# Optimization experiments

Hardware: AMD Instinct MI355X
Metric: run time of the kernel (lower is better)

## Reference

```python
import jax, jax.numpy as jnp
import numpy as np

T, B, DIM, N = 2048, 16, 1024, 64


def setup_inputs() -> dict:
    key = jax.random.key(0)
    ks = jax.random.split(key, 6)
    # xavier-uniform-ish scale for [N, DIM] linear weights
    lim = float(np.sqrt(6.0 / (DIM + N)))
    mk = lambda k: jax.random.uniform(k, (N, DIM), jnp.float32, -lim, lim)
    return {
        "x": jax.random.normal(ks[0], (T, B, DIM), jnp.float32),
        "S": jnp.zeros((B, N, N), jnp.float32),
        "W_k": mk(ks[1]),
        "W_v": mk(ks[2]),
        "W_q": mk(ks[3]),
        "W_alpha": mk(ks[4]),
        "d_alpha": jnp.full((N,), 0.1, jnp.float32),
        "b_alpha": jnp.full((N,), 2.0, jnp.float32),
    }


def reference(x, S, W_k, W_v, W_q, W_alpha, d_alpha, b_alpha):
    # Projections for the whole sequence at once: [T, B, N]
    k_all = jnp.einsum('tbd,nd->tbn', x, W_k)
    v_all = jnp.einsum('tbd,nd->tbn', x, W_v)
    q_all = jnp.einsum('tbd,nd->tbn', x, W_q)
    a_all = jnp.einsum('tbd,nd->tbn', x, W_alpha)

    def step(S, inp):
        k, v, q, ax = inp  # each [B, N]
        retrieved = jnp.einsum('bij,bj->bi', S, k)                 # [B, N]
        alpha = jax.nn.sigmoid(ax + d_alpha * retrieved + b_alpha)  # [B, N]
        outer_vk = v[:, :, None] * k[:, None, :]                    # [B, N, N]
        S = alpha[:, :, None] * S + (1.0 - alpha[:, :, None]) * outer_vk
        out = jnp.einsum('bij,bj->bi', S, q)                        # [B, N]
        out = out * jax.nn.silu(out)
        return S, out

    S_final, output = jax.lax.scan(step, S, (k_all, v_all, q_all, a_all))
    return output, S_final
```

## Files before the change

kernel.cpp:

```cpp
#include <hip/hip_runtime.h>
#include <hip/hip_bf16.h>

#define T_STEPS 2048
#define BATCH 16
#define DIM 1024
#define NDIM 64
#define M_TOTAL (T_STEPS * BATCH)
#define STRIDE (BATCH * NDIM)
#define CH 32
#define NC (T_STEPS / CH)

typedef __attribute__((ext_vector_type(8))) short bf16x8;
typedef __attribute__((ext_vector_type(4))) float f32x4;
typedef __attribute__((ext_vector_type(2))) float f32x2;

#define NEG_LOG2E -1.44269504088896f

__device__ inline unsigned pk_bf(float lo, float hi) {
    __hip_bfloat162 h = __float22bfloat162_rn(float2{lo, hi});
    return *(unsigned*)&h;
}

template <int CTRL>
__device__ inline float dpp_add(float x) {
    int v = __builtin_amdgcn_update_dpp(0, __float_as_int(x), CTRL, 0xF, 0xF, true);
    return x + __int_as_float(v);
}
__device__ inline float red16(float x) {
    x = dpp_add<0xB1>(x);
    x = dpp_add<0x4E>(x);
    x = dpp_add<0x141>(x);
    x = dpp_add<0x140>(x);
    return x;
}
__device__ inline void red16x2(float& a, float& b) {
    a = dpp_add<0xB1>(a);  b = dpp_add<0xB1>(b);
    a = dpp_add<0x4E>(a);  b = dpp_add<0x4E>(b);
    a = dpp_add<0x141>(a); b = dpp_add<0x141>(b);
    a = dpp_add<0x140>(a); b = dpp_add<0x140>(b);
}
__device__ inline float silu_o(float o) {
    float e = __builtin_amdgcn_exp2f(o * NEG_LOG2E);
    return o * o * __builtin_amdgcn_rcpf(1.f + e);
}

#define AS1 __attribute__((address_space(1)))
#define AS3 __attribute__((address_space(3)))
__device__ inline void gl_lds16(const float* g, float* l) {
    __builtin_amdgcn_global_load_lds((const AS1 unsigned*)g, (AS3 unsigned*)l, 16, 0, 0);
}
__device__ inline void gl_lds16s(const unsigned short* g, unsigned short* l) {
    __builtin_amdgcn_global_load_lds((const AS1 unsigned*)g, (AS3 unsigned*)l, 16, 0, 0);
}
__device__ inline void gl_lds4(const float* g, float* l) {
    __builtin_amdgcn_global_load_lds((const AS1 unsigned*)g, (AS3 unsigned*)l, 4, 0, 0);
}
#define WAIT_VM0 do { __builtin_amdgcn_s_waitcnt(0x0F70); asm volatile("" ::: "memory"); } while (0)

__global__ __launch_bounds__(256) void pack_w(
    const float* __restrict__ Wk, const float* __restrict__ Wq,
    const float* __restrict__ Wv, const float* __restrict__ Wa,
    unsigned short* __restrict__ Wb) {
    int n = blockIdx.x;
    int sel = n >> 6;
    const float* W = (sel == 0) ? Wk : (sel == 1) ? Wq : (sel == 2) ? Wv : Wa;
    int k4 = threadIdx.x * 4;
    float4 f = *(const float4*)(W + (size_t)(n & 63) * DIM + k4);
    uint2 u;
    u.x = pk_bf(f.x, f.y);
    u.y = pk_bf(f.z, f.w);
    *(uint2*)(Wb + (size_t)n * DIM + k4) = u;
}

__global__ __launch_bounds__(256, 2) void proj_kernel(
    const float* __restrict__ x, const unsigned short* __restrict__ Wb,
    const float* __restrict__ ba, float* __restrict__ Kp, float* __restrict__ Qp,
    float* __restrict__ VAi) {
    __shared__ float sA[128 * 64];
    __shared__ unsigned short sB[128 * 64];

    const int m0 = blockIdx.x * 128;
    const int ntile = blockIdx.y;
    const int tid = threadIdx.x;
    const int wv = tid >> 6, lane = tid & 63, lrow = lane & 15, quad = lane >> 4;
    const int wm = wv & 1, wn = wv >> 1;

    f32x4 acc[4][4];
#pragma unroll
    for (int a = 0; a < 4; a++)
#pragma unroll
        for (int b = 0; b < 4; b++) acc[a][b] = (f32x4)(0.f);

    const float* xg = x + (size_t)(m0 + (tid >> 4)) * DIM + (tid & 15) * 4;
    const unsigned short* wg = Wb + (size_t)(ntile * 128 + (tid >> 3)) * DIM + (tid & 7) * 8;

    for (int it = 0; it < 16; ++it) {
        const int k0 = it * 64;
        __syncthreads();
#pragma unroll
        for (int j = 0; j < 8; ++j)
            gl_lds16(xg + (size_t)(16 * j) * DIM + k0, &sA[(tid + 256 * j) * 4]);
#pragma unroll
        for (int j = 0; j < 4; ++j)
            gl_lds16s(wg + (size_t)(32 * j) * DIM + k0, &sB[(tid + 256 * j) * 8]);
        WAIT_VM0;
        __syncthreads();

#pragma unroll
        for (int ks = 0; ks < 2; ++ks) {
            bf16x8 af[4];
#pragma unroll
            for (int mt = 0; mt < 4; ++mt) {
                const float* pa = &sA[(wm * 64 + mt * 16 + lrow) * 64 + ks * 32 + quad * 8];
                float4 lo = ((const float4*)pa)[0], hi = ((const float4*)pa)[1];
                unsigned pk[4] = {pk_bf(lo.x, lo.y), pk_bf(lo.z, lo.w),
                                  pk_bf(hi.x, hi.y), pk_bf(hi.z, hi.w)};
                af[mt] = *(bf16x8*)pk;
            }
#pragma unroll
            for (int nt = 0; nt < 4; ++nt) {
                bf16x8 bfr = *(const bf16x8*)&sB[(wn * 64 + nt * 16 + lrow) * 64 + ks * 32 + quad * 8];
#pragma unroll
                for (int mt = 0; mt < 4; ++mt)
                    acc[mt][nt] = __builtin_amdgcn_mfma_f32_16x16x32_bf16(af[mt], bfr, acc[mt][nt], 0, 0, 0);
            }
        }
    }

    const int g2 = ntile * 2 + wn;
    float bav[4];
    if (g2 == 3) {
#pragma unroll
        for (int nt = 0; nt < 4; ++nt) bav[nt] = ba[nt * 16 + lrow];
    }
#pragma unroll
    for (int mt = 0; mt < 4; ++mt)
#pragma unroll
        for (int nt = 0; nt < 4; ++nt) {
            int col = nt * 16 + lrow;
#pragma unroll
            for (int reg = 0; reg < 4; ++reg) {
                int m = m0 + wm * 64 + mt * 16 + quad * 4 + reg;
                float vvv = acc[mt][nt][reg];
                if (g2 == 0) Kp[(size_t)m * 64 + col] = vvv;
                else if (g2 == 1) Qp[(size_t)m * 64 + col] = vvv;
                else if (g2 == 2) VAi[(size_t)m * 128 + col * 2] = vvv;
                else VAi[(size_t)m * 128 + col * 2 + 1] = NEG_LOG2E * (vvv + bav[nt]);
            }
        }
}

__global__ __launch_bounds__(256) void kq_kernel(
    const float* __restrict__ Kp, const float* __restrict__ Qp,
    float* __restrict__ kq, float* __restrict__ kk) {
    int m = blockIdx.x * 16 + (threadIdx.x >> 4);
    int c = threadIdx.x & 15;
    float4 k = *(const float4*)(Kp + (size_t)m * 64 + c * 4);
    float4 q = *(const float4*)(Qp + (size_t)m * 64 + c * 4);
    float4 kn = {0.f, 0.f, 0.f, 0.f};
    if (m + BATCH < M_TOTAL) kn = *(const float4*)(Kp + (size_t)(m + BATCH) * 64 + c * 4);
    float pq = k.x * q.x + k.y * q.y + k.z * q.z + k.w * q.w;
    float pk = k.x * kn.x + k.y * kn.y + k.z * kn.z + k.w * kn.w;
    red16x2(pq, pk);
    if (c == 0) { kq[m] = pq; kk[m] = pk; }
}

__global__ __launch_bounds__(64, 1) void recur_kernel(
    const float* __restrict__ Kp, const float* __restrict__ Qp,
    const float* __restrict__ VAi, const float* __restrict__ KQp,
    const float* __restrict__ KKp,
    const float* __restrict__ S0, const float* __restrict__ d_alpha,
    float* __restrict__ out, float* __restrict__ Sout) {
    __shared__ float Kl[2][CH][64];
    __shared__ float Ql[2][CH][64];
    __shared__ float VAl[2][CH][8];
    __shared__ float KQl[2][64];
    __shared__ float KKl[2][64];
    __shared__ float OlT[4][CH];

    int b = blockIdx.y, g = blockIdx.x, lane = threadIdx.x;
    int r = lane >> 4, c = lane & 15, i = g * 4 + r, c4 = c * 4;

    f32x4 sv = *(const f32x4*)(S0 + ((size_t)b * NDIM + i) * NDIM + c4);
    float da2 = d_alpha[i] * NEG_LOG2E;

    const float* Kbase = Kp + (size_t)b * NDIM + (size_t)(lane >> 4) * STRIDE + (lane & 15) * 4;
    const float* Qbase = Qp + (size_t)b * NDIM + (size_t)(lane >> 4) * STRIDE + (lane & 15) * 4;
    const float* VAbase = VAi + (size_t)b * 128 + g * 8 + (lane & 1) * 4 + (size_t)(lane >> 1) * 2048;
    const float* KQbase = KQp + b + (size_t)(lane & 31) * BATCH;
    const float* KKbase = KKp + b + (size_t)(lane & 31) * BATCH;

    auto load_chunk = [&](int t0, int buf) {
#pragma unroll
        for (int j = 0; j < 8; ++j) {
            gl_lds16(Kbase + (size_t)(t0 + j * 4) * STRIDE, &Kl[buf][j * 4][0]);
            gl_lds16(Qbase + (size_t)(t0 + j * 4) * STRIDE, &Ql[buf][j * 4][0]);
        }
        gl_lds16(VAbase + (size_t)t0 * 2048, &VAl[buf][0][0]);
        gl_lds4(KQbase + (size_t)t0 * BATCH, &KQl[buf][0]);
        gl_lds4(KKbase + (size_t)t0 * BATCH, &KKl[buf][0]);
    };

    f32x4 kg[2][4], qg[2][4], kqg[2], kkg[2];
    f32x2 vg[2][4];
    f32x4 og;
    float ee, ckm, rqm, vkk, vkq, v_cur;

#define LOADG(gi, buf, t4_) do {                                          \
    const float* Kb_ = &Kl[buf][0][0] + (t4_) * 64 + c4;                  \
    const float* Qb_ = &Ql[buf][0][0] + (t4_) * 64 + c4;                  \
    _Pragma("unroll")                                                     \
    for (int u_ = 0; u_ < 4; ++u_) {                                      \
        kg[gi][u_] = *(const f32x4*)(Kb_ + u_ * 64);                      \
        qg[gi][u_] = *(const f32x4*)(Qb_ + u_ * 64);                      \
        vg[gi][u_] = *(const f32x2*)(&VAl[buf][0][0] + ((t4_) + u_) * 8 + r * 2); \
    }                                                                     \
    kqg[gi] = *(const f32x4*)(&KQl[buf][0] + (t4_));                      \
    kkg[gi] = *(const f32x4*)(&KKl[buf][0] + (t4_));                      \
} while (0)

#define STEP(u, kt_, kt2_, qt1_, vt1_, kqt1_, kkt1_) do {                 \
    float alpha_ = __builtin_amdgcn_rcpf(1.f + ee);                       \
    float rk1_ = fmaf(alpha_, ckm, vkk);                 \
    ee = __builtin_amdgcn_exp2f(fmaf(da2, rk1_, (vt1_).y));               \
    float o_ = fmaf(alpha_, rqm, vkq);                       \
    f32x4 w_ = v_cur * (kt_);                                             \
    f32x4 d_ = sv - w_;                                                   \
    sv = w_ + alpha_ * d_;                                       \
    f32x2 pq_ = (qt1_).lo * sv.lo; pq_ = (qt1_).hi * sv.hi + pq_;         \
    f32x2 pk_ = (kt2_).lo * sv.lo; pk_ = (kt2_).hi * sv.hi + pk_;         \
    float rq_ = pq_.x + pq_.y, ck_ = pk_.x + pk_.y;                       \
    red16x2(rq_, ck_);                                  \
    float v1_ = (vt1_).x;                                                 \
    vkq = v1_ * (kqt1_); vkk = v1_ * (kkt1_);                             \
    rqm = rq_ - vkq; ckm = ck_ - vkk;                                     \
    og[u] = o_;                                                           \
    v_cur = v1_;                                                          \
} while (0)

#define GROUP_A() do {                                                          \
    STEP(0, kg[0][0], kg[0][2], qg[0][1], vg[0][1], kqg[0][1], kkg[0][1]);      \
    STEP(1, kg[0][1], kg[0][3], qg[0][2], vg[0][2], kqg[0][2], kkg[0][2]);      \
    STEP(2, kg[0][2], kg[1][0], qg[0][3], vg[0][3], kqg[0][3], kkg[0][3]);      \
    STEP(3, kg[0][3], kg[1][1], qg[1][0], vg[1][0], kqg[1][0], kkg[1][0]);      \
} while (0)
#define GROUP_B() do {                                                          \
    STEP(0, kg[1][0], kg[1][2], qg[1][1], vg[1][1], kqg[1][1], kkg[1][1]);      \
    STEP(1, kg[1][1], kg[1][3], qg[1][2], vg[1][2], kqg[1][2], kkg[1][2]);      \
    STEP(2, kg[1][2], kg[0][0], qg[1][3], vg[1][3], kqg[1][3], kkg[1][3]);      \
    STEP(3, kg[1][3], kg[0][1], qg[0][0], vg[0][0], kqg[0][0], kkg[0][0]);      \
} while (0)

    load_chunk(0, 0);
    WAIT_VM0;
    LOADG(0, 0, 0);
    {
        f32x2 p0 = kg[0][0].lo * sv.lo; p0 = kg[0][0].hi * sv.hi + p0;
        f32x2 p1 = qg[0][0].lo * sv.lo; p1 = qg[0][0].hi * sv.hi + p1;
        f32x2 p2 = kg[0][1].lo * sv.lo; p2 = kg[0][1].hi * sv.hi + p2;
        float rk0 = p0.x + p0.y, rq0 = p1.x + p1.y, ck0 = p2.x + p2.y;
        red16x2(rk0, rq0);
        ck0 = red16(ck0);
        float v0 = vg[0][0].x;
        ee = __builtin_amdgcn_exp2f(fmaf(da2, rk0, vg[0][0].y));
        vkq = v0 * kqg[0][0];
        vkk = v0 * kkg[0][0];
        rqm = rq0 - vkq;
        ckm = ck0 - vkk;
        v_cur = v0;
    }

#pragma unroll 1
    for (int j = 0; j < NC; ++j) {
        const int cb = j & 1, nb = cb ^ 1;
        if (j + 1 < NC) load_chunk((j + 1) * CH, nb);

#pragma unroll 1
        for (int t8 = 0; t8 < 24; t8 += 8) {
            LOADG(1, cb, t8 + 4);
            GROUP_A();
            if (c == 0) *(f32x4*)(&OlT[r][t8]) = og;
            LOADG(0, cb, t8 + 8);
            GROUP_B();
            if (c == 0) *(f32x4*)(&OlT[r][t8 + 4]) = og;
        }
        LOADG(1, cb, 28);
        GROUP_A();
        if (c == 0) *(f32x4*)(&OlT[r][24]) = og;
        WAIT_VM0;
        LOADG(0, nb, 0);
        GROUP_B();
        if (c == 0) *(f32x4*)(&OlT[r][28]) = og;

        if (lane < 32) {
            float4 t4o;
            t4o.x = silu_o(OlT[0][lane]);
            t4o.y = silu_o(OlT[1][lane]);
            t4o.z = silu_o(OlT[2][lane]);
            t4o.w = silu_o(OlT[3][lane]);
            *(float4*)(out + ((size_t)(j * CH + lane) * BATCH + b) * NDIM + g * 4) = t4o;
        }
    }
#undef GROUP_A
#undef GROUP_B
#undef STEP
#undef LOADG

    *(float4*)(Sout + ((size_t)b * NDIM + i) * NDIM + c4) = float4{sv.x, sv.y, sv.z, sv.w};
}

extern "C" void kernel_launch(void* const* d_in, const int* in_sizes, int n_in,
                              void* d_out, int out_size, void* d_ws, size_t ws_size,
                              hipStream_t stream) {
    const float* x  = (const float*)d_in[0];
    const float* S0 = (const float*)d_in[1];
    const float* Wk = (const float*)d_in[2];
    const float* Wv = (const float*)d_in[3];
    const float* Wq = (const float*)d_in[4];
    const float* Wa = (const float*)d_in[5];
    const float* da = (const float*)d_in[6];
    const float* ba = (const float*)d_in[7];

    float* out = (float*)d_out;
    float* Sout = out + (size_t)T_STEPS * BATCH * NDIM;

    const size_t per = (size_t)M_TOTAL * NDIM;
    float* Kp  = (float*)d_ws;
    float* Qp  = Kp + per;
    float* VAi = Qp + per;
    float* kq  = VAi + 2 * per;
    float* kk  = kq + M_TOTAL;
    unsigned short* Wb = (unsigned short*)(kk + M_TOTAL);

    pack_w<<<dim3(256), dim3(256), 0, stream>>>(Wk, Wq, Wv, Wa, Wb);
    proj_kernel<<<dim3(M_TOTAL / 128, 2), dim3(256), 0, stream>>>(x, Wb, ba, Kp, Qp, VAi);
    kq_kernel<<<dim3(M_TOTAL / 16), dim3(256), 0, stream>>>(Kp, Qp, kq, kk);
    recur_kernel<<<dim3(16, BATCH), dim3(64), 0, stream>>>(Kp, Qp, VAi, kq, kk, S0, da, out, Sout);
}
```

Measured before the change: 446.1 us.

## Widen projection tile to all four weights and defer output reduction in recurrence

The projection kernel now computes all 256 output columns per block, one weight matrix per wave, so each x tile is loaded and converted to bf16 only once instead of twice. This raises accumulator registers to 32 MFMA tiles per wave and doubles the shared memory for weights, which may lower occupancy. In the recurrence, the per-step q-readout no longer goes through a cross-lane reduction on the critical path. Instead each lane keeps an unreduced partial output, using the previous step's partial q·S together with a precomputed correction term, and four steps' outputs are reduced in one batched DPP pass. This removes one reduction chain per step from the serial dependency.

```diff
diff --git a/kernel.cpp b/kernel.cpp
--- a/kernel.cpp
+++ b/kernel.cpp
@@ -38,6 +38,12 @@
     a = dpp_add<0x4E>(a);  b = dpp_add<0x4E>(b);
     a = dpp_add<0x141>(a); b = dpp_add<0x141>(b);
     a = dpp_add<0x140>(a); b = dpp_add<0x140>(b);
+}
+__device__ inline void red16x4(float& a, float& b, float& cc, float& d) {
+    a = dpp_add<0xB1>(a);  b = dpp_add<0xB1>(b);  cc = dpp_add<0xB1>(cc);  d = dpp_add<0xB1>(d);
+    a = dpp_add<0x4E>(a);  b = dpp_add<0x4E>(b);  cc = dpp_add<0x4E>(cc);  d = dpp_add<0x4E>(d);
+    a = dpp_add<0x141>(a); b = dpp_add<0x141>(b); cc = dpp_add<0x141>(cc); d = dpp_add<0x141>(d);
+    a = dpp_add<0x140>(a); b = dpp_add<0x140>(b); cc = dpp_add<0x140>(cc); d = dpp_add<0x140>(d);
 }
 __device__ inline float silu_o(float o) {
     float e = __builtin_amdgcn_exp2f(o * NEG_LOG2E);
@@ -77,22 +83,20 @@
     const float* __restrict__ ba, float* __restrict__ Kp, float* __restrict__ Qp,
     float* __restrict__ VAi) {
     __shared__ float sA[128 * 64];
-    __shared__ unsigned short sB[128 * 64];
+    __shared__ unsigned short sB[256 * 64];
 
     const int m0 = blockIdx.x * 128;
-    const int ntile = blockIdx.y;
     const int tid = threadIdx.x;
     const int wv = tid >> 6, lane = tid & 63, lrow = lane & 15, quad = lane >> 4;
-    const int wm = wv & 1, wn = wv >> 1;
-
-    f32x4 acc[4][4];
-#pragma unroll
-    for (int a = 0; a < 4; a++)
+
+    f32x4 acc[8][4];
+#pragma unroll
+    for (int a = 0; a < 8; a++)
 #pragma unroll
         for (int b = 0; b < 4; b++) acc[a][b] = (f32x4)(0.f);
 
     const float* xg = x + (size_t)(m0 + (tid >> 4)) * DIM + (tid & 15) * 4;
-    const unsigned short* wg = Wb + (size_t)(ntile * 128 + (tid >> 3)) * DIM + (tid & 7) * 8;
+    const unsigned short* wg = Wb + (size_t)(tid >> 3) * DIM + (tid & 7) * 8;
 
     for (int it = 0; it < 16; ++it) {
         const int k0 = it * 64;
@@ -101,17 +105,17 @@
         for (int j = 0; j < 8; ++j)
             gl_lds16(xg + (size_t)(16 * j) * DIM + k0, &sA[(tid + 256 * j) * 4]);
 #pragma unroll
-        for (int j = 0; j < 4; ++j)
+        for (int j = 0; j < 8; ++j)
             gl_lds16s(wg + (size_t)(32 * j) * DIM + k0, &sB[(tid + 256 * j) * 8]);
         WAIT_VM0;
         __syncthreads();
 
 #pragma unroll
         for (int ks = 0; ks < 2; ++ks) {
-            bf16x8 af[4];
-#pragma unroll
-            for (int mt = 0; mt < 4; ++mt) {
-                const float* pa = &sA[(wm * 64 + mt * 16 + lrow) * 64 + ks * 32 + quad * 8];
+            bf16x8 af[8];
+#pragma unroll
+            for (int mt = 0; mt < 8; ++mt) {
+                const float* pa = &sA[(mt * 16 + lrow) * 64 + ks * 32 + quad * 8];
                 float4 lo = ((const float4*)pa)[0], hi = ((const float4*)pa)[1];
                 unsigned pk[4] = {pk_bf(lo.x, lo.y), pk_bf(lo.z, lo.w),
                                   pk_bf(hi.x, hi.y), pk_bf(hi.z, hi.w)};
@@ -119,28 +123,28 @@
             }
 #pragma unroll
             for (int nt = 0; nt < 4; ++nt) {
-                bf16x8 bfr = *(const bf16x8*)&sB[(wn * 64 + nt * 16 + lrow) * 64 + ks * 32 + quad * 8];
-#pragma unroll
-                for (int mt = 0; mt < 4; ++mt)
+                bf16x8 bfr = *(const bf16x8*)&sB[(wv * 64 + nt * 16 + lrow) * 64 + ks * 32 + quad * 8];
+#pragma unroll
+                for (int mt = 0; mt < 8; ++mt)
                     acc[mt][nt] = __builtin_amdgcn_mfma_f32_16x16x32_bf16(af[mt], bfr, acc[mt][nt], 0, 0, 0);
             }
         }
     }
 
-    const int g2 = ntile * 2 + wn;
+    const int g2 = wv;
     float bav[4];
     if (g2 == 3) {
 #pragma unroll
         for (int nt = 0; nt < 4; ++nt) bav[nt] = ba[nt * 16 + lrow];
     }
 #pragma unroll
-    for (int mt = 0; mt < 4; ++mt)
+    for (int mt = 0; mt < 8; ++mt)
 #pragma unroll
         for (int nt = 0; nt < 4; ++nt) {
             int col = nt * 16 + lrow;
 #pragma unroll
             for (int reg = 0; reg < 4; ++reg) {
-                int m = m0 + wm * 64 + mt * 16 + quad * 4 + reg;
+                int m = m0 + mt * 16 + quad * 4 + reg;
                 float vvv = acc[mt][nt][reg];
                 if (g2 == 0) Kp[(size_t)m * 64 + col] = vvv;
                 else if (g2 == 1) Qp[(size_t)m * 64 + col] = vvv;
@@ -203,8 +207,8 @@
 
     f32x4 kg[2][4], qg[2][4], kqg[2], kkg[2];
     f32x2 vg[2][4];
-    f32x4 og;
-    float ee, ckm, rqm, vkk, vkq, v_cur;
+    float og_0, og_1, og_2, og_3;
+    float ee, ckm, vkk, vkq, v_cur, pqprev;
 
 #define LOADG(gi, buf, t4_) do {                                          \
     const float* Kb_ = &Kl[buf][0][0] + (t4_) * 64 + c4;                  \
@@ -223,32 +227,36 @@
     float alpha_ = __builtin_amdgcn_rcpf(1.f + ee);                       \
     float rk1_ = fmaf(alpha_, ckm, vkk);                 \
     ee = __builtin_amdgcn_exp2f(fmaf(da2, rk1_, (vt1_).y));               \
-    float o_ = fmaf(alpha_, rqm, vkq);                       \
-    f32x4 w_ = v_cur * (kt_);                                             \
-    f32x4 d_ = sv - w_;                                                   \
-    sv = w_ + alpha_ * d_;                                       \
+    float om_ = 1.f - alpha_;                                             \
+    og_##u = fmaf(alpha_, pqprev, om_ * vkq * 0.0625f);   \
+    float beta_ = om_ * v_cur;                                            \
+    sv = alpha_ * sv + beta_ * (kt_);                            \
     f32x2 pq_ = (qt1_).lo * sv.lo; pq_ = (qt1_).hi * sv.hi + pq_;         \
     f32x2 pk_ = (kt2_).lo * sv.lo; pk_ = (kt2_).hi * sv.hi + pk_;         \
-    float rq_ = pq_.x + pq_.y, ck_ = pk_.x + pk_.y;                       \
-    red16x2(rq_, ck_);                                  \
+    pqprev = pq_.x + pq_.y;                                               \
+    float ck_ = pk_.x + pk_.y;                                            \
+    ck_ = red16(ck_);                              \
     float v1_ = (vt1_).x;                                                 \
     vkq = v1_ * (kqt1_); vkk = v1_ * (kkt1_);                             \
-    rqm = rq_ - vkq; ckm = ck_ - vkk;                                     \
-    og[u] = o_;                                                           \
+    ckm = ck_ - vkk;                                                      \
     v_cur = v1_;                                                          \
 } while (0)
 
-#define GROUP_A() do {                                                          \
+#define GROUP_A(t8_) do {                                                       \
     STEP(0, kg[0][0], kg[0][2], qg[0][1], vg[0][1], kqg[0][1], kkg[0][1]);      \
     STEP(1, kg[0][1], kg[0][3], qg[0][2], vg[0][2], kqg[0][2], kkg[0][2]);      \
     STEP(2, kg[0][2], kg[1][0], qg[0][3], vg[0][3], kqg[0][3], kkg[0][3]);      \
     STEP(3, kg[0][3], kg[1][1], qg[1][0], vg[1][0], kqg[1][0], kkg[1][0]);      \
+    red16x4(og_0, og_1, og_2, og_3);                                            \
+    if (c == 0) *(f32x4*)(&OlT[r][t8_]) = (f32x4){og_0, og_1, og_2, og_3};      \
 } while (0)
-#define GROUP_B() do {                                                          \
+#define GROUP_B(t8_) do {                                                       \
     STEP(0, kg[1][0], kg[1][2], qg[1][1], vg[1][1], kqg[1][1], kkg[1][1]);      \
     STEP(1, kg[1][1], kg[1][3], qg[1][2], vg[1][2], kqg[1][2], kkg[1][2]);      \
     STEP(2, kg[1][2], kg[0][0], qg[1][3], vg[1][3], kqg[1][3], kkg[1][3]);      \
     STEP(3, kg[1][3], kg[0][1], qg[0][0], vg[0][0], kqg[0][0], kkg[0][0]);      \
+    red16x4(og_0, og_1, og_2, og_3);                                            \
+    if (c == 0) *(f32x4*)(&OlT[r][t8_]) = (f32x4){og_0, og_1, og_2, og_3};      \
 } while (0)
 
     load_chunk(0, 0);
@@ -258,14 +266,13 @@
         f32x2 p0 = kg[0][0].lo * sv.lo; p0 = kg[0][0].hi * sv.hi + p0;
         f32x2 p1 = qg[0][0].lo * sv.lo; p1 = qg[0][0].hi * sv.hi + p1;
         f32x2 p2 = kg[0][1].lo * sv.lo; p2 = kg[0][1].hi * sv.hi + p2;
-        float rk0 = p0.x + p0.y, rq0 = p1.x + p1.y, ck0 = p2.x + p2.y;
-        red16x2(rk0, rq0);
-        ck0 = red16(ck0);
+        float rk0 = p0.x + p0.y, ck0 = p2.x + p2.y;
+        pqprev = p1.x + p1.y;
+        red16x2(rk0, ck0);
         float v0 = vg[0][0].x;
         ee = __builtin_amdgcn_exp2f(fmaf(da2, rk0, vg[0][0].y));
         vkq = v0 * kqg[0][0];
         vkk = v0 * kkg[0][0];
-        rqm = rq0 - vkq;
         ckm = ck0 - vkk;
         v_cur = v0;
     }
@@ -278,19 +285,15 @@
 #pragma unroll 1
         for (int t8 = 0; t8 < 24; t8 += 8) {
             LOADG(1, cb, t8 + 4);
-            GROUP_A();
-            if (c == 0) *(f32x4*)(&OlT[r][t8]) = og;
+            GROUP_A(t8);
             LOADG(0, cb, t8 + 8);
-            GROUP_B();
-            if (c == 0) *(f32x4*)(&OlT[r][t8 + 4]) = og;
+            GROUP_B(t8 + 4);
         }
         LOADG(1, cb, 28);
-        GROUP_A();
-        if (c == 0) *(f32x4*)(&OlT[r][24]) = og;
+        GROUP_A(24);
         WAIT_VM0;
         LOADG(0, nb, 0);
-        GROUP_B();
-        if (c == 0) *(f32x4*)(&OlT[r][28]) = og;
+        GROUP_B(28);
 
         if (lane < 32) {
             float4 t4o;
@@ -333,7 +336,7 @@
     unsigned short* Wb = (unsigned short*)(kk + M_TOTAL);
 
     pack_w<<<dim3(256), dim3(256), 0, stream>>>(Wk, Wq, Wv, Wa, Wb);
-    proj_kernel<<<dim3(M_TOTAL / 128, 2), dim3(256), 0, stream>>>(x, Wb, ba, Kp, Qp, VAi);
+    proj_kernel<<<dim3(M_TOTAL / 128), dim3(256), 0, stream>>>(x, Wb, ba, Kp, Qp, VAi);
     kq_kernel<<<dim3(M_TOTAL / 16), dim3(256), 0, stream>>>(Kp, Qp, kq, kk);
     recur_kernel<<<dim3(16, BATCH), dim3(64), 0, stream>>>(Kp, Qp, VAi, kq, kk, S0, da, out, Sout);
 }
```

New measurement: 470.0 us. 1.05x slower.
